# Performance work log

Hardware: AMD Instinct MI355X
Metric: run time of the kernel (lower is better)

## Reference

```python
import jax, jax.numpy as jnp
from jax import lax
import numpy as np

B, E, K, CAP = 512, 16, 2, 64
H = W = 32
ALPHA, LOAD_PEN, MIN_USE, RTEMP = 0.7, 2.0, 0.05, 1.0


def _conv(x, w, b):
    y = lax.conv_general_dilated(x, w, (1, 1), 'SAME', dimension_numbers=('NCHW', 'OIHW', 'NCHW'))
    return y + b[None, :, None, None]


def _bn(x, s, b):
    # eval-mode BatchNorm2d: running_mean=0, running_var=1 folded into scale/bias
    return x * s[None, :, None, None] + b[None, :, None, None]


def _ln(x, g, b, eps=1e-5):
    m = x.mean(-1, keepdims=True)
    v = ((x - m) ** 2).mean(-1, keepdims=True)
    return (x - m) * lax.rsqrt(v + eps) * g + b


def _maxpool(x):
    return lax.reduce_window(x, -jnp.inf, lax.max, (1, 1, 2, 2), (1, 1, 2, 2), 'VALID')


def setup_inputs() -> dict:
    key = jax.random.key(0)
    ks = iter(jax.random.split(key, 64))

    def nrm(shape, fan_in):
        return jax.random.normal(next(ks), shape, jnp.float32) / float(np.sqrt(fan_in))

    inp = {'x': jax.random.normal(next(ks), (B, 3, H, W), jnp.float32)}
    for i, (ci, co) in enumerate([(3, 64), (64, 64), (64, 128), (128, 128), (128, 256), (256, 256)], 1):
        inp[f'conv_w{i}'] = nrm((co, ci, 3, 3), ci * 9)
        inp[f'conv_b{i}'] = jnp.zeros((co,), jnp.float32)
        inp[f'bn_s{i}'] = jnp.ones((co,), jnp.float32)
        inp[f'bn_b{i}'] = jnp.zeros((co,), jnp.float32)
    inp['gate_w1'] = nrm((E, 64, 256), 256); inp['gate_b1'] = jnp.zeros((E, 64)); inp['gate_g1'] = jnp.ones((E, 64)); inp['gate_bb1'] = jnp.zeros((E, 64))
    inp['gate_w2'] = nrm((E, 32, 64), 64); inp['gate_b2'] = jnp.zeros((E, 32))
    inp['gate_w3'] = nrm((E, 1, 32), 32); inp['gate_b3'] = jnp.zeros((E, 1))
    inp['exp_w1'] = nrm((E, 256, 256), 256); inp['exp_b1'] = jnp.zeros((E, 256)); inp['exp_g1'] = jnp.ones((E, 256)); inp['exp_bb1'] = jnp.zeros((E, 256))
    inp['exp_w2'] = nrm((E, 128, 256), 256); inp['exp_b2'] = jnp.zeros((E, 128)); inp['exp_g2'] = jnp.ones((E, 128)); inp['exp_bb2'] = jnp.zeros((E, 128))
    inp['exp_w3'] = nrm((E, 128, 128), 128); inp['exp_b3'] = jnp.zeros((E, 128))
    inp['cls_w'] = nrm((E, 10, 128), 128); inp['cls_b'] = jnp.zeros((E, 10))
    return inp


def _forward(x, conv_w1, conv_b1, bn_s1, bn_b1, conv_w2, conv_b2, bn_s2, bn_b2,
             conv_w3, conv_b3, bn_s3, bn_b3, conv_w4, conv_b4, bn_s4, bn_b4,
             conv_w5, conv_b5, bn_s5, bn_b5, conv_w6, conv_b6, bn_s6, bn_b6,
             gate_w1, gate_b1, gate_g1, gate_bb1, gate_w2, gate_b2, gate_w3, gate_b3,
             exp_w1, exp_b1, exp_g1, exp_bb1, exp_w2, exp_b2, exp_g2, exp_bb2,
             exp_w3, exp_b3, cls_w, cls_b):
    # ---- trunk (eval: dropout = identity) ----
    h = jax.nn.relu(_bn(_conv(x, conv_w1, conv_b1), bn_s1, bn_b1))
    h = jax.nn.relu(_bn(_conv(h, conv_w2, conv_b2), bn_s2, bn_b2))
    h = _maxpool(h)
    h = jax.nn.relu(_bn(_conv(h, conv_w3, conv_b3), bn_s3, bn_b3))
    h = jax.nn.relu(_bn(_conv(h, conv_w4, conv_b4), bn_s4, bn_b4))
    h = _maxpool(h)
    h = jax.nn.relu(_bn(_conv(h, conv_w5, conv_b5), bn_s5, bn_b5))
    h = jax.nn.relu(_bn(_conv(h, conv_w6, conv_b6), bn_s6, bn_b6))
    feats = h.mean((2, 3))  # AdaptiveAvgPool2d(1) + Flatten -> [B, 256]
    # ---- experts (vectorized over E) ----
    h1 = jax.nn.relu(_ln(jnp.einsum('bc,eoc->beo', feats, exp_w1) + exp_b1, exp_g1, exp_bb1))
    h2 = jax.nn.relu(_ln(jnp.einsum('beh,eoh->beo', h1, exp_w2) + exp_b2, exp_g2, exp_bb2))
    embeds = jnp.einsum('beh,eoh->beo', h2, exp_w3) + exp_b3  # [B, E, 128]
    logits_e = jnp.einsum('bed,ecd->bec', embeds, cls_w) + cls_b  # [B, E, 10]
    probs = jax.nn.softmax(logits_e, axis=2)
    entropy = -(probs * jnp.log(probs + 1e-12)).sum(-1)  # [B, E]
    confidence = -entropy
    # ---- gates (vectorized over E) ----
    g1 = jax.nn.relu(_ln(jnp.einsum('bc,eoc->beo', feats, gate_w1) + gate_b1, gate_g1, gate_bb1))
    g2 = jax.nn.relu(jnp.einsum('beh,eoh->beo', g1, gate_w2) + gate_b2)
    scores = (jnp.einsum('beh,eoh->beo', g2, gate_w3) + gate_b3)[..., 0] / RTEMP  # [B, E]
    # ---- top-k capacity routing (eval: usage_ema at init = 1/E, no noise) ----
    usage = jnp.full((E,), 1.0 / E, jnp.float32)
    combined = ALPHA * scores + (1.0 - ALPHA) * confidence
    combined = combined + jnp.where(usage < MIN_USE, (MIN_USE - usage) * 10.0, 0.0)[None, :]
    balanced = combined - LOAD_PEN * usage[None, :]
    _, topk_idx = lax.top_k(balanced, K)  # [B, K]

    def step(loads, idx_row):
        lt = loads[idx_row]  # [K]
        avail = lt < CAP
        chosen = jnp.where(jnp.any(avail), idx_row[jnp.argmax(avail)], idx_row[jnp.argmin(lt)])
        return loads.at[chosen].add(1.0), chosen

    _, chosen = lax.scan(step, jnp.zeros((E,), jnp.float32), topk_idx)
    D = jax.nn.one_hot(chosen, E, dtype=jnp.bool_)  # [B, E]
    masked = jnp.where(D, balanced, -jnp.inf)
    rw = jax.nn.softmax(masked, axis=1) * D
    rw = rw / (rw.sum(1, keepdims=True) + 1e-12)
    final_logits = jnp.einsum('be,bec->bc', rw, logits_e)
    return final_logits, balanced, D


def reference(x, conv_w1, conv_b1, bn_s1, bn_b1, conv_w2, conv_b2, bn_s2, bn_b2,
              conv_w3, conv_b3, bn_s3, bn_b3, conv_w4, conv_b4, bn_s4, bn_b4,
              conv_w5, conv_b5, bn_s5, bn_b5, conv_w6, conv_b6, bn_s6, bn_b6,
              gate_w1, gate_b1, gate_g1, gate_bb1, gate_w2, gate_b2, gate_w3, gate_b3,
              exp_w1, exp_b1, exp_g1, exp_bb1, exp_w2, exp_b2, exp_g2, exp_bb2,
              exp_w3, exp_b3, cls_w, cls_b):
    return _forward(x, conv_w1, conv_b1, bn_s1, bn_b1, conv_w2, conv_b2, bn_s2, bn_b2,
                    conv_w3, conv_b3, bn_s3, bn_b3, conv_w4, conv_b4, bn_s4, bn_b4,
                    conv_w5, conv_b5, bn_s5, bn_b5, conv_w6, conv_b6, bn_s6, bn_b6,
                    gate_w1, gate_b1, gate_g1, gate_bb1, gate_w2, gate_b2, gate_w3, gate_b3,
                    exp_w1, exp_b1, exp_g1, exp_bb1, exp_w2, exp_b2, exp_g2, exp_bb2,
                    exp_w3, exp_b3, cls_w, cls_b)
```

## Files before the change

### kernel.cpp

```cpp
#include <hip/hip_runtime.h>


typedef _Float16 h16;
typedef _Float16 half8 __attribute__((ext_vector_type(8)));
typedef float f32x16 __attribute__((ext_vector_type(16)));

__device__ __forceinline__ void split2f(float x, h16& hh, h16& ll) {
  h16 a = (h16)x;
  hh = a;
  ll = (h16)(x - (float)a);
}

__device__ __forceinline__ void dma_b16(const h16* g, h16* l) {
  __builtin_amdgcn_global_load_lds(
      (const __attribute__((address_space(1))) void*)g,
      (__attribute__((address_space(3))) void*)l, 16, 0, 0);
}

__global__ void prep_all_k(const float* __restrict__ cw1, const float* __restrict__ cw2,
                           const float* __restrict__ cw3, const float* __restrict__ cw4,
                           const float* __restrict__ cw5, const float* __restrict__ cw6,
                           float* __restrict__ wt1t, h16* __restrict__ wh,
                           h16* p0, h16* p1, h16* p2, h16* p3) {
  int idx = blockIdx.x * 256 + threadIdx.x;
  if (idx < 64) {
    h16* p = (idx < 16) ? p0 : (idx < 32) ? p1 : (idx < 48) ? p2 : p3;
    p[idx & 15] = (h16)0.f;
    return;
  }
  idx -= 64;
  if (idx < 1728) {
    int co = idx % 64, r = idx / 64;
    wt1t[idx] = cw1[(size_t)co * 27 + r];
    return;
  }
  idx -= 1728;
  const float* w; int CIN, COUT; size_t off;
  if (idx < 36864)        { w = cw2; CIN = 64;  COUT = 64;  off = 0; }
  else if (idx < 110592)  { w = cw3; CIN = 64;  COUT = 128; off = 36864;  idx -= 36864; }
  else if (idx < 258048)  { w = cw4; CIN = 128; COUT = 128; off = 110592; idx -= 110592; }
  else if (idx < 552960)  { w = cw5; CIN = 128; COUT = 256; off = 258048; idx -= 258048; }
  else if (idx < 1142784) { w = cw6; CIN = 256; COUT = 256; off = 552960; idx -= 552960; }
  else return;
  int KCOB = COUT >> 6;
  int lidx = idx;
  int c8   = idx & 7;
  int t    = idx >> 3;
  int co64 = t & 63;  t >>= 6;
  int half = t & 1;   t >>= 1;
  int cob  = t % KCOB; t /= KCOB;
  int tap  = t % 9;
  int ck   = t / 9;
  int ci = ck * 16 + half * 8 + c8;
  int co = cob * 64 + co64;
  float v = w[((size_t)co * CIN + ci) * 9 + tap];
  wh[off + lidx] = (h16)v;
}

__global__ __launch_bounds__(256) void conv1_k(
    const float* __restrict__ x, const float* __restrict__ wt,
    const float* __restrict__ cb, const float* __restrict__ bns,
    const float* __restrict__ bnb, h16* __restrict__ oh, h16* __restrict__ ol)
{
  __shared__ float sx[3 * 34 * 34];
  const int tid = threadIdx.x;
  const int img = blockIdx.x;
  for (int idx = tid; idx < 3 * 34 * 34; idx += 256) {
    int xx = idx % 34;
    int t  = idx / 34;
    int rr = t % 34;
    int c  = t / 34;
    int gr = rr - 1, gx = xx - 1;
    float v = 0.f;
    if (gr >= 0 && gr < 32 && gx >= 0 && gx < 32)
      v = x[((size_t)(img * 3 + c) * 32 + gr) * 32 + gx];
    sx[(c * 34 + rr) * 34 + xx] = v;
  }
  __syncthreads();
#pragma unroll 1
  for (int k = 0; k < 4; ++k) {
    int px = k * 256 + tid;
    int yy = px >> 5, xx = px & 31;
    float in27[27];
#pragma unroll
    for (int c = 0; c < 3; ++c)
#pragma unroll
      for (int dy = 0; dy < 3; ++dy)
#pragma unroll
        for (int dx = 0; dx < 3; ++dx)
          in27[c * 9 + dy * 3 + dx] = sx[(c * 34 + yy + dy) * 34 + xx + dx];
#pragma unroll 1
    for (int cbk = 0; cbk < 4; ++cbk) {
      h16 hb[16], lb[16];
#pragma unroll
      for (int j = 0; j < 16; ++j) {
        int co = cbk * 16 + j;
        float acc = 0.f;
#pragma unroll
        for (int t = 0; t < 27; ++t) acc = fmaf(in27[t], wt[t * 64 + co], acc);
        float s = bns[co];
        float yv = fmaxf(fmaf(acc + cb[co], s, bnb[co]), 0.f);
        split2f(yv, hb[j], lb[j]);
      }
      size_t o = 16 + ((size_t)(img * 4 + cbk) * 1024 + px) * 16;
      *(half8*)&oh[o]     = *(half8*)&hb[0];
      *(half8*)&oh[o + 8] = *(half8*)&hb[8];
      *(half8*)&ol[o]     = *(half8*)&lb[0];
      *(half8*)&ol[o + 8] = *(half8*)&lb[8];
    }
  }
}

template<int H, int W, int CIN, int COUT, int MT, int POOL, int OCC, int DBUF>
__global__ __launch_bounds__(256, OCC) void conv_mfma(
    const h16* __restrict__ Ah, const h16* __restrict__ Al,
    const h16* __restrict__ Wh,
    const float* __restrict__ cb, const float* __restrict__ bns,
    const float* __restrict__ bnb,
    h16* __restrict__ Oh, h16* __restrict__ Ol, float* __restrict__ feats)
{
  constexpr int TPI  = (H * W) / 32;
  constexpr int RPT  = 32 / W;
  constexpr int IPB  = (4 * MT * 32 >= H * W) ? (4 * MT * 32) / (H * W) : 1;
  constexpr int KC   = CIN / 16;
  constexpr int HW   = H * W;
  constexpr int KCO  = COUT / 16;
  constexpr int KCOB = COUT / 64;
  constexpr int LOGW = (W == 32) ? 5 : (W == 16) ? 4 : 3;
  constexpr int ROWS_COV = (4 * MT * 32) / (W * IPB);
  constexpr int ROFF  = (ROWS_COV < H) ? 1 : 0;
  constexpr int SROWS = ROWS_COV + 2 * ROFF;
  constexpr int ASZ = IPB * SROWS * W * 16;
  constexpr int ACH = ASZ / 8;
  constexpr int ACH2 = ACH / 2;
  constexpr int HSPLIT = (ROFF == 0) ? 1 : 0;
  constexpr int NBUF = DBUF ? 2 : 1;
  constexpr int TCH  = 1152 + 2 * ACH;
  constexpr int NI   = (TCH + 255) / 256;

  __shared__ h16 sB[NBUF][9 * 2 * 64 * 8];
  __shared__ h16 sA[NBUF][2][ASZ + 16];

  const int tid  = threadIdx.x;
  const int lane = tid & 63;
  const int wave = tid >> 6;
  const int half = lane >> 5;
  const int col  = lane & 31;
  const int cob  = blockIdx.z;
  const int co0  = cob * 64;
  const int r0img = blockIdx.y * ROWS_COV;

  auto STAGE = [&](int ck, int nb) {
#pragma unroll
    for (int i = 0; i < NI; ++i) {
      int id = tid + i * 256;
      if (id < 1152) {
        int src = ((ck * 9 + (id >> 7)) * KCOB + cob) * 1024 + (id & 127) * 8;
        dma_b16(Wh + src, &sB[nb][id * 8]);
      } else if (id < TCH) {
        int c2 = id - 1152;
        int pl = c2 / ACH;
        int cc = c2 - pl * ACH;
        if constexpr (HSPLIT) {
          int hs  = cc / ACH2;
          int px  = cc - hs * ACH2;
          int iL  = px / (SROWS * W);
          int rem = px - iL * (SROWS * W);
          int rs  = rem / W;
          int pxx = rem - rs * W;
          int grow = r0img + rs;
          const h16* gp = pl ? Al : Ah;
          int srcA = 16 + (((blockIdx.x * IPB + iL) * KC + ck) * HW + grow * W + pxx) * 16 + hs * 8;
          dma_b16(gp + srcA, &sA[nb][pl][cc * 8]);
        } else {
          int hs  = cc & 1;
          int pxg = cc >> 1;
          int iL  = pxg / (SROWS * W);
          int rem = pxg - iL * (SROWS * W);
          int rs  = rem / W;
          int px  = rem - rs * W;
          int grow = r0img + rs - ROFF;
          if (ROFF == 0 || ((unsigned)grow < (unsigned)H)) {
            const h16* gp = pl ? Al : Ah;
            int srcA = 16 + (((blockIdx.x * IPB + iL) * KC + ck) * HW + grow * W + px) * 16 + hs * 8;
            dma_b16(gp + srcA, &sA[nb][pl][cc * 8]);
          }
        }
      }
    }
  };

  int scc[MT], ty[MT], tx[MT], img_t[MT], rw0[MT];
#pragma unroll
  for (int t = 0; t < MT; ++t) {
    int gt   = blockIdx.y * (4 * MT) + wave * MT + t;
    int imgL = (gt / TPI) % IPB;
    int img  = blockIdx.x * IPB + gt / TPI;
    int row0 = (gt % TPI) * RPT;
    int y = row0 + (col >> LOGW);
    int x = col & (W - 1);
    img_t[t] = img; rw0[t] = row0; ty[t] = y; tx[t] = x;
    if constexpr (HSPLIT)
      scc[t] = half * ACH2 + (imgL * SROWS + (y - r0img)) * W + x;
    else
      scc[t] = ((imgL * SROWS + (y - r0img + ROFF)) * W + x) * 16 + half * 8;
  }

  f32x16 acc[MT][2];
#pragma unroll
  for (int t = 0; t < MT; ++t)
#pragma unroll
    for (int n = 0; n < 2; ++n)
#pragma unroll
      for (int i = 0; i < 16; ++i) acc[t][n][i] = 0.f;

  if (tid < NBUF * 2 * 16) {
    int wsl = tid >> 4;
    sA[wsl >> 1][wsl & 1][ASZ + (tid & 15)] = (h16)0.f;
  }
  STAGE(0, 0);
  __syncthreads();

  const int zoff = ASZ + half * 8;

  int buf = 0;
#pragma unroll 1
  for (int ck = 0; ck < KC; ++ck) {
    if constexpr (DBUF) {
      if (ck + 1 < KC) STAGE(ck + 1, buf ^ 1);
    }
    const h16* bB = &sB[buf][0];
    const h16* aH = &sA[buf][0][0];
    const h16* aL = &sA[buf][1][0];

#pragma unroll
    for (int tap = 0; tap < 9; ++tap) {
      const int dy = tap / 3 - 1, dx = tap % 3 - 1;
      const int dsh = dy * W + dx;
      half8 bh[2];
#pragma unroll
      for (int n = 0; n < 2; ++n)
        bh[n] = *(const half8*)&bB[((tap * 2 + half) * 64 + n * 32 + col) * 8];
      half8 ah[MT], al[MT];
#pragma unroll
      for (int t = 0; t < MT; ++t) {
        bool v = ((unsigned)(ty[t] + dy) < (unsigned)H) &&
                 ((unsigned)(tx[t] + dx) < (unsigned)W);
        int po;
        if constexpr (HSPLIT) po = v ? ((scc[t] + dsh) * 8) : zoff;
        else                  po = v ? (scc[t] + dsh * 16) : zoff;
        ah[t] = *(const half8*)(aH + po);
        al[t] = *(const half8*)(aL + po);
      }
#pragma unroll
      for (int t = 0; t < MT; ++t)
#pragma unroll
        for (int n = 0; n < 2; ++n) {
          acc[t][n] = __builtin_amdgcn_mfma_f32_32x32x16_f16(ah[t], bh[n], acc[t][n], 0, 0, 0);
          acc[t][n] = __builtin_amdgcn_mfma_f32_32x32x16_f16(al[t], bh[n], acc[t][n], 0, 0, 0);
        }
    }

    if constexpr (DBUF) {
      __syncthreads();
      buf ^= 1;
    } else {
      __syncthreads();
      if (ck + 1 < KC) {
        STAGE(ck + 1, 0);
        __syncthreads();
      }
    }
  }

#pragma unroll
  for (int n = 0; n < 2; ++n) {
    const int co = co0 + n * 32 + col;
    const float es = bns[co];
    const float eb = fmaf(cb[co], es, bnb[co]);
    const int cko = co >> 4, c16 = co & 15;

    if constexpr (POOL == 0) {
#pragma unroll
      for (int t = 0; t < MT; ++t) {
#pragma unroll
        for (int r = 0; r < 16; ++r) {
          float v = fmaxf(fmaf(acc[t][n][r], es, eb), 0.f);
          int m = (r & 3) + 4 * half + 8 * (r >> 2);
          int y = rw0[t] + (m >> LOGW);
          int x = m & (W - 1);
          size_t oi = 16 + ((size_t)(img_t[t] * KCO + cko) * HW + y * W + x) * 16 + c16;
          h16 hh, ll; split2f(v, hh, ll);
          Oh[oi] = hh; Ol[oi] = ll;
        }
      }
    } else if constexpr (POOL == 1 && RPT == 1) {
      constexpr int HWq = (H / 2) * (W / 2);
#pragma unroll
      for (int tp = 0; tp < MT / 2; ++tp) {
        const int t0 = 2 * tp, t1 = 2 * tp + 1;
        const int yq = rw0[t0] >> 1;
#pragma unroll
        for (int r = 0; r < 16; r += 2) {
          float v00 = fmaxf(fmaf(acc[t0][n][r],     es, eb), 0.f);
          float v01 = fmaxf(fmaf(acc[t0][n][r + 1], es, eb), 0.f);
          float v10 = fmaxf(fmaf(acc[t1][n][r],     es, eb), 0.f);
          float v11 = fmaxf(fmaf(acc[t1][n][r + 1], es, eb), 0.f);
          float mv = fmaxf(fmaxf(v00, v01), fmaxf(v10, v11));
          int xq = ((r & 3) >> 1) + 2 * half + 4 * (r >> 2);
          size_t oi = 16 + ((size_t)(img_t[t0] * KCO + cko) * HWq + yq * (W / 2) + xq) * 16 + c16;
          h16 hh, ll; split2f(mv, hh, ll);
          Oh[oi] = hh; Ol[oi] = ll;
        }
      }
    } else if constexpr (POOL == 1) {
      constexpr int HWq = (H / 2) * (W / 2);
#pragma unroll
      for (int t = 0; t < MT; ++t) {
        const int yq = rw0[t] >> 1;
#pragma unroll
        for (int r = 0; r < 8; r += 2) {
          float v00 = fmaxf(fmaf(acc[t][n][r],     es, eb), 0.f);
          float v01 = fmaxf(fmaf(acc[t][n][r + 1], es, eb), 0.f);
          float v10 = fmaxf(fmaf(acc[t][n][r + 8], es, eb), 0.f);
          float v11 = fmaxf(fmaf(acc[t][n][r + 9], es, eb), 0.f);
          float mv = fmaxf(fmaxf(v00, v01), fmaxf(v10, v11));
          int xq = ((r & 3) >> 1) + 2 * half + 4 * (r >> 2);
          size_t oi = 16 + ((size_t)(img_t[t] * KCO + cko) * HWq + yq * (W / 2) + xq) * 16 + c16;
          h16 hh, ll; split2f(mv, hh, ll);
          Oh[oi] = hh; Ol[oi] = ll;
        }
      }
    } else if constexpr (POOL == 2 && MT == 1) {
      float* sRd = (float*)&sA[0][0][0];
      float s = 0.f;
#pragma unroll
      for (int r = 0; r < 16; ++r)
        s += fmaxf(fmaf(acc[0][n][r], es, eb), 0.f);
      s += __shfl_xor(s, 32, 64);
      if (half == 0) sRd[wave * 64 + n * 32 + col] = s;
    } else if constexpr (POOL == 2) {
      float s = 0.f;
#pragma unroll
      for (int t = 0; t < MT; ++t)
#pragma unroll
        for (int r = 0; r < 16; ++r)
          s += fmaxf(fmaf(acc[t][n][r], es, eb), 0.f);
      s += __shfl_xor(s, 32, 64);
      if (half == 0) feats[(size_t)img_t[0] * 256 + co] = s * (1.f / 64.f);
    }
  }

  if constexpr (POOL == 2 && MT == 1) {
    float* sRd = (float*)&sA[0][0][0];
    __syncthreads();
    if (tid < 128) {
      int li = tid >> 6, co_l = tid & 63;
      float s = sRd[(li * 2) * 64 + co_l] + sRd[(li * 2 + 1) * 64 + co_l];
      feats[(size_t)(blockIdx.x * 2 + li) * 256 + co0 + co_l] = s * (1.f / 64.f);
    }
  }
}

template<int O, int K, int LN, int RELU>
__global__ __launch_bounds__(256, 4) void gemm_head(
    const float* __restrict__ A, size_t aStrideE,
    const float* __restrict__ Wm, const float* __restrict__ bias,
    const float* __restrict__ g, const float* __restrict__ bb,
    float* __restrict__ out)
{
  constexpr int KC  = (O >= 256) ? 32 : 64;
  constexpr int WST = O + 4;
  constexpr int TO  = O / 16;
  __shared__ float sA[KC * 36];
  __shared__ float sW[KC * WST];
  __shared__ float mArr[32], rArr[32];

  const int tid  = threadIdx.x;
  const int lane = tid & 63;
  const int wave = tid >> 6;
  const int e    = blockIdx.y;
  const int b0g  = blockIdx.x * 32;
  const int bl   = (lane & 15) * 2;
  const int ol   = wave * (O / 4) + (lane >> 4) * TO;

  const float* Ae = A + (size_t)e * aStrideE;
  const float* We = Wm + (size_t)e * O * K;

  float acc[2][TO];
#pragma unroll
  for (int i = 0; i < 2; ++i)
#pragma unroll
    for (int j = 0; j < TO; ++j) acc[i][j] = 0.f;

  for (int k0 = 0; k0 < K; k0 += KC) {
    for (int idx = tid; idx < 32 * KC; idx += 256) {
      int kk = idx % KC, bb_ = idx / KC;
      sA[kk * 36 + bb_] = Ae[(size_t)(b0g + bb_) * K + k0 + kk];
    }
    for (int idx = tid; idx < O * KC; idx += 256) {
      int kk = idx % KC, oo = idx / KC;
      sW[kk * WST + oo] = We[(size_t)oo * K + k0 + kk];
    }
    __syncthreads();
#pragma unroll 4
    for (int kk = 0; kk < KC; ++kk) {
      float2 av = *(const float2*)&sA[kk * 36 + bl];
      float a2[2] = {av.x, av.y};
#pragma unroll
      for (int j4 = 0; j4 < TO; j4 += 4) {
        float4 wv = *(const float4*)&sW[kk * WST + ol + j4];
        float w4[4] = {wv.x, wv.y, wv.z, wv.w};
#pragma unroll
        for (int i = 0; i < 2; ++i)
#pragma unroll
          for (int jj = 0; jj < 4; ++jj)
            acc[i][j4 + jj] = fmaf(a2[i], w4[jj], acc[i][j4 + jj]);
      }
    }
    __syncthreads();
  }

  const float* bi = bias + (size_t)e * O;
#pragma unroll
  for (int i = 0; i < 2; ++i)
#pragma unroll
    for (int j = 0; j < TO; ++j) acc[i][j] += bi[ol + j];

  if constexpr (LN) {
    float* redS = sA;
    float* redQ = sA + 512;
    const int grp = wave * 4 + (lane >> 4);
#pragma unroll
    for (int i = 0; i < 2; ++i) {
      float s = 0.f, q = 0.f;
#pragma unroll
      for (int j = 0; j < TO; ++j) { s += acc[i][j]; q += acc[i][j] * acc[i][j]; }
      redS[(bl + i) * 16 + grp] = s;
      redQ[(bl + i) * 16 + grp] = q;
    }
    __syncthreads();
    if (tid < 32) {
      float s = 0.f, q = 0.f;
#pragma unroll
      for (int gi = 0; gi < 16; ++gi) { s += redS[tid * 16 + gi]; q += redQ[tid * 16 + gi]; }
      float mean = s * (1.f / O);
      float var  = q * (1.f / O) - mean * mean;
      mArr[tid] = mean;
      rArr[tid] = rsqrtf(var + 1e-5f);
    }
    __syncthreads();
    const float* gp  = g + (size_t)e * O;
    const float* bbp = bb + (size_t)e * O;
#pragma unroll
    for (int i = 0; i < 2; ++i) {
      float mean = mArr[bl + i], rstd = rArr[bl + i];
#pragma unroll
      for (int j = 0; j < TO; ++j)
        acc[i][j] = (acc[i][j] - mean) * rstd * gp[ol + j] + bbp[ol + j];
    }
  }
  if constexpr (RELU) {
#pragma unroll
    for (int i = 0; i < 2; ++i)
#pragma unroll
      for (int j = 0; j < TO; ++j) acc[i][j] = fmaxf(acc[i][j], 0.f);
  }
#pragma unroll
  for (int i = 0; i < 2; ++i) {
    float* op = out + ((size_t)e * 512 + b0g + bl + i) * O + ol;
#pragma unroll
    for (int j4 = 0; j4 < TO; j4 += 4)
      *(float4*)(op + j4) = make_float4(acc[i][j4], acc[i][j4 + 1], acc[i][j4 + 2], acc[i][j4 + 3]);
  }
}

__global__ void heads_small_k(const float* __restrict__ embeds,
                              const float* __restrict__ cw,
                              const float* __restrict__ cbias,
                              const float* __restrict__ g1, const float* __restrict__ w2,
                              const float* __restrict__ b2, const float* __restrict__ w3,
                              const float* __restrict__ b3,
                              float* __restrict__ logits_e, float* __restrict__ conf,
                              float* __restrict__ scores)
{
  int wv   = (blockIdx.x * 256 + threadIdx.x) >> 6;
  int lane = threadIdx.x & 63;
  int b = wv >> 4, e = wv & 15;

  const float* ep = embeds + ((size_t)e * 512 + b) * 128;
  float e0 = ep[lane], e1 = ep[lane + 64];
  float l[10];
#pragma unroll
  for (int o = 0; o < 10; ++o) {
    const float* wp = cw + ((size_t)e * 10 + o) * 128;
    l[o] = e0 * wp[lane] + e1 * wp[lane + 64];
  }
#pragma unroll
  for (int s = 32; s >= 1; s >>= 1)
#pragma unroll
    for (int o = 0; o < 10; ++o) l[o] += __shfl_xor(l[o], s, 64);
#pragma unroll
  for (int o = 0; o < 10; ++o) l[o] += cbias[e * 10 + o];
  float m = l[0];
#pragma unroll
  for (int o = 1; o < 10; ++o) m = fmaxf(m, l[o]);
  float p[10], sum = 0.f;
#pragma unroll
  for (int o = 0; o < 10; ++o) { p[o] = expf(l[o] - m); sum += p[o]; }
  float inv = 1.f / sum, ent = 0.f;
#pragma unroll
  for (int o = 0; o < 10; ++o) { float pp = p[o] * inv; ent -= pp * logf(pp + 1e-12f); }
  if (lane == 0) {
    conf[b * 16 + e] = -ent;
#pragma unroll
    for (int o = 0; o < 10; ++o) logits_e[((size_t)b * 16 + e) * 10 + o] = l[o];
  }

  float gv = g1[((size_t)e * 512 + b) * 64 + lane];
  const float* w3p = w3 + e * 32;
  float sc = 0.f;
#pragma unroll
  for (int o = 0; o < 32; ++o) {
    float t = gv * w2[((size_t)e * 32 + o) * 64 + lane];
#pragma unroll
    for (int s = 32; s >= 1; s >>= 1) t += __shfl_xor(t, s, 64);
    float g2v = fmaxf(t + b2[e * 32 + o], 0.f);
    sc = fmaf(g2v, w3p[o], sc);
  }
  if (lane == 0) scores[b * 16 + e] = sc + b3[e];
}

__global__ void routing_k(const float* __restrict__ scores, const float* __restrict__ conf,
                          const float* __restrict__ logits_e, float* __restrict__ out)
{
  __shared__ int t2[512];
  __shared__ int chs[512];
  const int tid = threadIdx.x;

  if (tid < 512) {
    int b = tid;
    float v0 = -3.4e38f, v1 = -3.4e38f;
    int i0 = 0, i1 = 0;
#pragma unroll
    for (int e = 0; e < 16; ++e) {
      float s = scores[b * 16 + e];
      float c = conf[b * 16 + e];
      float v = 0.7f * s + 0.3f * c - 0.125f;
      out[5120 + b * 16 + e] = v;
      if (v > v0) { v1 = v0; i1 = i0; v0 = v; i0 = e; }
      else if (v > v1) { v1 = v; i1 = e; }
    }
    t2[b] = i0 | (i1 << 8);
  }
  __syncthreads();

  if (tid < 64) {
    int lane = tid;
    int cnt = 0;
    int pk[8];
#pragma unroll
    for (int k = 0; k < 8; ++k) pk[k] = t2[k * 64 + lane];
#pragma unroll 1
    for (int k = 0; k < 8; ++k) {
      for (int j = 0; j < 64; ++j) {
        int pair = __shfl(pk[k], j, 64);
        int i0 = pair & 0xff, i1 = (pair >> 8) & 0xff;
        int c0 = __shfl(cnt, i0, 64);
        int c1 = __shfl(cnt, i1, 64);
        int ch = (c0 < 64) ? i0 : ((c1 < 64) ? i1 : ((c0 <= c1) ? i0 : i1));
        cnt += (lane == ch) ? 1 : 0;
        if (lane == 0) chs[k * 64 + j] = ch;
      }
    }
  }
  __syncthreads();

  if (tid < 512) {
    int b = tid;
    int ch = chs[b];
#pragma unroll
    for (int e = 0; e < 16; ++e)
      out[13312 + b * 16 + e] = (e == ch) ? 1.0f : 0.0f;
#pragma unroll
    for (int o = 0; o < 10; ++o)
      out[b * 10 + o] = logits_e[((size_t)b * 16 + ch) * 10 + o];
  }
}

extern "C" void kernel_launch(void* const* d_in, const int* in_sizes, int n_in,
                              void* d_out, int out_size, void* d_ws, size_t ws_size,
                              hipStream_t stream) {
  (void)in_sizes; (void)n_in; (void)out_size; (void)ws_size;

  const float* x = (const float*)d_in[0];
  const float *cw[6], *cbv[6], *bsv[6], *bbv[6];
  for (int i = 0; i < 6; ++i) {
    cw[i]  = (const float*)d_in[1 + 4 * i];
    cbv[i] = (const float*)d_in[2 + 4 * i];
    bsv[i] = (const float*)d_in[3 + 4 * i];
    bbv[i] = (const float*)d_in[4 + 4 * i];
  }
  const float* gate_w1  = (const float*)d_in[25];
  const float* gate_b1  = (const float*)d_in[26];
  const float* gate_g1  = (const float*)d_in[27];
  const float* gate_bb1 = (const float*)d_in[28];
  const float* gate_w2  = (const float*)d_in[29];
  const float* gate_b2  = (const float*)d_in[30];
  const float* gate_w3  = (const float*)d_in[31];
  const float* gate_b3  = (const float*)d_in[32];
  const float* exp_w1   = (const float*)d_in[33];
  const float* exp_b1   = (const float*)d_in[34];
  const float* exp_g1   = (const float*)d_in[35];
  const float* exp_bb1  = (const float*)d_in[36];
  const float* exp_w2   = (const float*)d_in[37];
  const float* exp_b2   = (const float*)d_in[38];
  const float* exp_g2   = (const float*)d_in[39];
  const float* exp_bb2  = (const float*)d_in[40];
  const float* exp_w3   = (const float*)d_in[41];
  const float* exp_b3   = (const float*)d_in[42];
  const float* cls_w    = (const float*)d_in[43];
  const float* cls_b    = (const float*)d_in[44];

  char* wsb = (char*)d_ws;
  const size_t off_wt1t = 0;
  const size_t off_whi  = 6912;
  const size_t off_Phi  = 4578048;
  const size_t off_Plo  = 71687168;
  const size_t off_Qhi  = 138796288;
  const size_t off_Qlo  = 155573760;
  const size_t off_feats= 172351232;
  const size_t off_h1   = 138796288 + 512;
  const size_t off_h2   = off_h1 + 8388608;
  const size_t off_emb  = off_h2 + 4194304;
  const size_t off_g1   = off_emb + 4194304;
  const size_t off_lg   = off_g1 + 2097152;
  const size_t off_conf = off_lg + 327680;
  const size_t off_sc   = off_conf + 32768;

  float* wt1t = (float*)(wsb + off_wt1t);
  h16* whi = (h16*)(wsb + off_whi);
  h16* Phi = (h16*)(wsb + off_Phi);
  h16* Plo = (h16*)(wsb + off_Plo);
  h16* Qhi = (h16*)(wsb + off_Qhi);
  h16* Qlo = (h16*)(wsb + off_Qlo);
  float* feats = (float*)(wsb + off_feats);
  float* h1 = (float*)(wsb + off_h1);
  float* h2 = (float*)(wsb + off_h2);
  float* emb = (float*)(wsb + off_emb);
  float* g1 = (float*)(wsb + off_g1);
  float* lg = (float*)(wsb + off_lg);
  float* conf = (float*)(wsb + off_conf);
  float* sc = (float*)(wsb + off_sc);

  const size_t wo2 = 0;
  const size_t wo3 = 36864;
  const size_t wo4 = 110592;
  const size_t wo5 = 258048;
  const size_t wo6 = 552960;

  prep_all_k<<<4471, 256, 0, stream>>>(cw[0], cw[1], cw[2], cw[3], cw[4], cw[5],
                                       wt1t, whi, Phi, Plo, Qhi, Qlo);

  conv1_k<<<512, 256, 0, stream>>>(x, wt1t, cbv[0], bsv[0], bbv[0], Phi, Plo);
  conv_mfma<32, 32, 64, 64, 2, 1, 3, 0><<<dim3(512, 4, 1), 256, 0, stream>>>(
      Phi, Plo, whi + wo2, cbv[1], bsv[1], bbv[1], Qhi, Qlo, nullptr);
  conv_mfma<16, 16, 64, 128, 2, 0, 3, 0><<<dim3(512, 1, 2), 256, 0, stream>>>(
      Qhi, Qlo, whi + wo3, cbv[2], bsv[2], bbv[2], Phi, Plo, nullptr);
  conv_mfma<16, 16, 128, 128, 2, 1, 3, 0><<<dim3(512, 1, 2), 256, 0, stream>>>(
      Phi, Plo, whi + wo4, cbv[3], bsv[3], bbv[3], Qhi, Qlo, nullptr);
  conv_mfma<8, 8, 128, 256, 2, 0, 3, 0><<<dim3(128, 1, 4), 256, 0, stream>>>(
      Qhi, Qlo, whi + wo5, cbv[4], bsv[4], bbv[4], Phi, Plo, nullptr);
  conv_mfma<8, 8, 256, 256, 2, 2, 3, 0><<<dim3(128, 1, 4), 256, 0, stream>>>(
      Phi, Plo, whi + wo6, cbv[5], bsv[5], bbv[5], nullptr, nullptr, feats);

  gemm_head<256, 256, 1, 1><<<dim3(16, 16), 256, 0, stream>>>(
      feats, (size_t)0, exp_w1, exp_b1, exp_g1, exp_bb1, h1);
  gemm_head<64, 256, 1, 1><<<dim3(16, 16), 256, 0, stream>>>(
      feats, (size_t)0, gate_w1, gate_b1, gate_g1, gate_bb1, g1);
  gemm_head<128, 256, 1, 1><<<dim3(16, 16), 256, 0, stream>>>(
      h1, (size_t)512 * 256, exp_w2, exp_b2, exp_g2, exp_bb2, h2);
  gemm_head<128, 128, 0, 0><<<dim3(16, 16), 256, 0, stream>>>(
      h2, (size_t)512 * 128, exp_w3, exp_b3, nullptr, nullptr, emb);
  heads_small_k<<<2048, 256, 0, stream>>>(emb, cls_w, cls_b,
                                          g1, gate_w2, gate_b2, gate_w3, gate_b3,
                                          lg, conf, sc);

  routing_k<<<1, 512, 0, stream>>>(sc, conf, lg, (float*)d_out);
}
```

Measured before the change: 746.2 us.

## Load conv weights directly from global into registers for 8x8 layers

Adds a BREG template mode in which the MFMA conv kernel reads the weight fragments for each tap straight from global memory into registers instead of staging them through LDS. Only the activation tiles are copied into shared memory. The two 8x8 conv layers switch to this mode with MT=1, double buffering and twice as many blocks, which cuts LDS use and adds parallelism. In exchange, the weight loads now sit on the critical path, depend on the cache for reuse, and give less reuse per block.

```diff
diff --git a/kernel.cpp b/kernel.cpp
--- a/kernel.cpp
+++ b/kernel.cpp
@@ -111,7 +111,7 @@
   }
 }
 
-template<int H, int W, int CIN, int COUT, int MT, int POOL, int OCC, int DBUF>
+template<int H, int W, int CIN, int COUT, int MT, int POOL, int OCC, int DBUF, int BREG>
 __global__ __launch_bounds__(256, OCC) void conv_mfma(
     const h16* __restrict__ Ah, const h16* __restrict__ Al,
     const h16* __restrict__ Wh,
@@ -135,10 +135,12 @@
   constexpr int ACH2 = ACH / 2;
   constexpr int HSPLIT = (ROFF == 0) ? 1 : 0;
   constexpr int NBUF = DBUF ? 2 : 1;
-  constexpr int TCH  = 1152 + 2 * ACH;
+  constexpr int TCH  = BREG ? (2 * ACH) : (1152 + 2 * ACH);
   constexpr int NI   = (TCH + 255) / 256;
-
-  __shared__ h16 sB[NBUF][9 * 2 * 64 * 8];
+  constexpr int SBH  = 9 * 2 * 64 * 8;
+  constexpr int SBSZ = BREG ? 8 : (NBUF * SBH);
+
+  __shared__ h16 sB[SBSZ];
   __shared__ h16 sA[NBUF][2][ASZ + 16];
 
   const int tid  = threadIdx.x;
@@ -150,41 +152,48 @@
   const int co0  = cob * 64;
   const int r0img = blockIdx.y * ROWS_COV;
 
+  auto stageA = [&](int ck, int nb, int cc2) {
+    int pl = cc2 / ACH;
+    int cc = cc2 - pl * ACH;
+    if constexpr (HSPLIT) {
+      int hs  = cc / ACH2;
+      int px  = cc - hs * ACH2;
+      int iL  = px / (SROWS * W);
+      int rem = px - iL * (SROWS * W);
+      int rs  = rem / W;
+      int pxx = rem - rs * W;
+      int grow = r0img + rs;
+      const h16* gp = pl ? Al : Ah;
+      int srcA = 16 + (((blockIdx.x * IPB + iL) * KC + ck) * HW + grow * W + pxx) * 16 + hs * 8;
+      dma_b16(gp + srcA, &sA[nb][pl][cc * 8]);
+    } else {
+      int hs  = cc & 1;
+      int pxg = cc >> 1;
+      int iL  = pxg / (SROWS * W);
+      int rem = pxg - iL * (SROWS * W);
+      int rs  = rem / W;
+      int px  = rem - rs * W;
+      int grow = r0img + rs - ROFF;
+      if (ROFF == 0 || ((unsigned)grow < (unsigned)H)) {
+        const h16* gp = pl ? Al : Ah;
+        int srcA = 16 + (((blockIdx.x * IPB + iL) * KC + ck) * HW + grow * W + px) * 16 + hs * 8;
+        dma_b16(gp + srcA, &sA[nb][pl][cc * 8]);
+      }
+    }
+  };
+
   auto STAGE = [&](int ck, int nb) {
 #pragma unroll
     for (int i = 0; i < NI; ++i) {
       int id = tid + i * 256;
-      if (id < 1152) {
-        int src = ((ck * 9 + (id >> 7)) * KCOB + cob) * 1024 + (id & 127) * 8;
-        dma_b16(Wh + src, &sB[nb][id * 8]);
-      } else if (id < TCH) {
-        int c2 = id - 1152;
-        int pl = c2 / ACH;
-        int cc = c2 - pl * ACH;
-        if constexpr (HSPLIT) {
-          int hs  = cc / ACH2;
-          int px  = cc - hs * ACH2;
-          int iL  = px / (SROWS * W);
-          int rem = px - iL * (SROWS * W);
-          int rs  = rem / W;
-          int pxx = rem - rs * W;
-          int grow = r0img + rs;
-          const h16* gp = pl ? Al : Ah;
-          int srcA = 16 + (((blockIdx.x * IPB + iL) * KC + ck) * HW + grow * W + pxx) * 16 + hs * 8;
-          dma_b16(gp + srcA, &sA[nb][pl][cc * 8]);
-        } else {
-          int hs  = cc & 1;
-          int pxg = cc >> 1;
-          int iL  = pxg / (SROWS * W);
-          int rem = pxg - iL * (SROWS * W);
-          int rs  = rem / W;
-          int px  = rem - rs * W;
-          int grow = r0img + rs - ROFF;
-          if (ROFF == 0 || ((unsigned)grow < (unsigned)H)) {
-            const h16* gp = pl ? Al : Ah;
-            int srcA = 16 + (((blockIdx.x * IPB + iL) * KC + ck) * HW + grow * W + px) * 16 + hs * 8;
-            dma_b16(gp + srcA, &sA[nb][pl][cc * 8]);
-          }
+      if constexpr (BREG) {
+        if (id < TCH) stageA(ck, nb, id);
+      } else {
+        if (id < 1152) {
+          int src = ((ck * 9 + (id >> 7)) * KCOB + cob) * 1024 + (id & 127) * 8;
+          dma_b16(Wh + src, &sB[nb * SBH + id * 8]);
+        } else if (id < TCH) {
+          stageA(ck, nb, id - 1152);
         }
       }
     }
@@ -229,18 +238,25 @@
     if constexpr (DBUF) {
       if (ck + 1 < KC) STAGE(ck + 1, buf ^ 1);
     }
-    const h16* bB = &sB[buf][0];
+    const h16* bB = &sB[BREG ? 0 : (buf * SBH)];
     const h16* aH = &sA[buf][0][0];
     const h16* aL = &sA[buf][1][0];
+    const h16* bG = Wh + ((size_t)ck * 9 * KCOB + cob) * 1024 + half * 512;
 
 #pragma unroll
     for (int tap = 0; tap < 9; ++tap) {
       const int dy = tap / 3 - 1, dx = tap % 3 - 1;
       const int dsh = dy * W + dx;
       half8 bh[2];
-#pragma unroll
-      for (int n = 0; n < 2; ++n)
-        bh[n] = *(const half8*)&bB[((tap * 2 + half) * 64 + n * 32 + col) * 8];
+      if constexpr (BREG) {
+        const h16* bt = bG + (size_t)tap * KCOB * 1024;
+        bh[0] = *(const half8*)&bt[col * 8];
+        bh[1] = *(const half8*)&bt[(32 + col) * 8];
+      } else {
+#pragma unroll
+        for (int n = 0; n < 2; ++n)
+          bh[n] = *(const half8*)&bB[((tap * 2 + half) * 64 + n * 32 + col) * 8];
+      }
       half8 ah[MT], al[MT];
 #pragma unroll
       for (int t = 0; t < MT; ++t) {
@@ -663,15 +679,15 @@
                                        wt1t, whi, Phi, Plo, Qhi, Qlo);
 
   conv1_k<<<512, 256, 0, stream>>>(x, wt1t, cbv[0], bsv[0], bbv[0], Phi, Plo);
-  conv_mfma<32, 32, 64, 64, 2, 1, 3, 0><<<dim3(512, 4, 1), 256, 0, stream>>>(
+  conv_mfma<32, 32, 64, 64, 2, 1, 3, 0, 0><<<dim3(512, 4, 1), 256, 0, stream>>>(
       Phi, Plo, whi + wo2, cbv[1], bsv[1], bbv[1], Qhi, Qlo, nullptr);
-  conv_mfma<16, 16, 64, 128, 2, 0, 3, 0><<<dim3(512, 1, 2), 256, 0, stream>>>(
+  conv_mfma<16, 16, 64, 128, 2, 0, 3, 0, 0><<<dim3(512, 1, 2), 256, 0, stream>>>(
       Qhi, Qlo, whi + wo3, cbv[2], bsv[2], bbv[2], Phi, Plo, nullptr);
-  conv_mfma<16, 16, 128, 128, 2, 1, 3, 0><<<dim3(512, 1, 2), 256, 0, stream>>>(
+  conv_mfma<16, 16, 128, 128, 2, 1, 3, 0, 0><<<dim3(512, 1, 2), 256, 0, stream>>>(
       Phi, Plo, whi + wo4, cbv[3], bsv[3], bbv[3], Qhi, Qlo, nullptr);
-  conv_mfma<8, 8, 128, 256, 2, 0, 3, 0><<<dim3(128, 1, 4), 256, 0, stream>>>(
+  conv_mfma<8, 8, 128, 256, 1, 0, 3, 1, 1><<<dim3(256, 1, 4), 256, 0, stream>>>(
       Qhi, Qlo, whi + wo5, cbv[4], bsv[4], bbv[4], Phi, Plo, nullptr);
-  conv_mfma<8, 8, 256, 256, 2, 2, 3, 0><<<dim3(128, 1, 4), 256, 0, stream>>>(
+  conv_mfma<8, 8, 256, 256, 1, 2, 3, 1, 1><<<dim3(256, 1, 4), 256, 0, stream>>>(
       Phi, Plo, whi + wo6, cbv[5], bsv[5], bbv[5], nullptr, nullptr, feats);
 
   gemm_head<256, 256, 1, 1><<<dim3(16, 16), 256, 0, stream>>>(
```

New measurement: 688.0 us. -7.8%, faster.
